# Optimization experiments

Measured on AMD Instinct MI355X. Metric: run time of the kernel, lower is better.

Reference implementation:

```python
import jax, jax.numpy as jnp
import numpy as np

N_NODES = 100000
N_EDGES = 3200000
D_IN = 128
D_OUT = 128
BN_EPS = 1e-5


def setup_inputs() -> dict:
    key = jax.random.key(0)
    k1, k2, k3, k4, k5 = jax.random.split(key, 5)
    x = jax.random.normal(k1, (N_NODES, D_IN), dtype=jnp.float32)
    edge_index = jax.random.randint(k2, (2, N_EDGES), 0, N_NODES, dtype=jnp.int64)
    s = 1.0 / np.sqrt(D_IN)
    W_l = jax.random.uniform(k3, (D_IN, D_OUT), minval=-s, maxval=s, dtype=jnp.float32)
    b_l = jnp.zeros((D_OUT,), dtype=jnp.float32)
    W_r = jax.random.uniform(k4, (D_IN, D_OUT), minval=-s, maxval=s, dtype=jnp.float32)
    gamma = jnp.ones((D_OUT,), dtype=jnp.float32)
    beta = jnp.zeros((D_OUT,), dtype=jnp.float32)
    return {"x": x, "edge_index": edge_index, "W_l": W_l, "b_l": b_l,
            "W_r": W_r, "gamma": gamma, "beta": beta}


def _sage_bn(x, edge_index, W_l, b_l, W_r, gamma, beta):
    src, dst = edge_index[0], edge_index[1]
    # gather source features, scatter-sum at targets, divide by in-degree (mean aggr)
    agg_sum = jax.ops.segment_sum(x[src], dst, num_segments=N_NODES)  # [N, D_IN]
    deg = jax.ops.segment_sum(jnp.ones((N_EDGES,), x.dtype), dst, num_segments=N_NODES)
    agg = agg_sum / jnp.maximum(deg, 1.0)[:, None]
    # SAGEConv: lin_l(aggregated) + lin_r(self)
    x_raw = agg @ W_l + b_l + x @ W_r  # [N, D_OUT]
    # BatchNorm1d (training mode: batch stats, biased variance)
    mu = jnp.mean(x_raw, axis=0)
    var = jnp.var(x_raw, axis=0)
    x_deskewed = (x_raw - mu) * jax.lax.rsqrt(var + BN_EPS) * gamma + beta
    return x_raw, x_deskewed


def reference(x, edge_index, W_l, b_l, W_r, gamma, beta):
    return _sage_bn(x, edge_index, W_l, b_l, W_r, gamma, beta)
```

## Files before the change

kernel.cpp:

```cpp
#include <hip/hip_runtime.h>

constexpr int NN = 100000;
constexpr int NE = 3200000;
constexpr int DD = 128;
constexpr int NB = 782;
constexpr int RND = 8192;
#define BN_EPS 1e-5f

typedef __attribute__((ext_vector_type(8))) short bf16x8;
typedef __attribute__((ext_vector_type(4))) float f32x4;
typedef __attribute__((ext_vector_type(2))) float f32x2;

constexpr size_t WS_CNT   = 0;
constexpr size_t WS_COFF  = 4096;
constexpr size_t WS_CUR   = 8192;
constexpr size_t WS_FLAG  = 12288;
constexpr size_t WS_BNSUM = 12800;
constexpr size_t WS_BNSQ  = 13312;
constexpr size_t WS_ZERO  = 16384;
constexpr size_t WS_DEG   = 16384;
constexpr size_t WS_OFF   = 416384;
constexpr size_t WS_CSR   = 816384;
constexpr size_t WS_WT    = 13616384;

__device__ inline unsigned bf16rne(float f) {
    unsigned u = __float_as_uint(f);
    return (u + 0x7fffu + ((u >> 16) & 1u)) >> 16;
}

#if __has_builtin(__builtin_amdgcn_cvt_pk_f32_fp8)
__device__ inline f32x2 fp8pk_lo(unsigned u) {
    return __builtin_amdgcn_cvt_pk_f32_fp8((int)u, false);
}
__device__ inline f32x2 fp8pk_hi(unsigned u) {
    return __builtin_amdgcn_cvt_pk_f32_fp8((int)u, true);
}
__device__ inline unsigned f32x4_to_fp8(float4 v) {
    int w = __builtin_amdgcn_cvt_pk_fp8_f32(v.x, v.y, 0, false);
    w = __builtin_amdgcn_cvt_pk_fp8_f32(v.z, v.w, w, true);
    return (unsigned)w;
}
#else
__device__ inline float fp8_to_f32_1(unsigned b) {
    unsigned s = (b & 0x80u) << 24;
    unsigned em = b & 0x7fu;
    float f;
    if (em >= 8) f = __uint_as_float((em << 20) + (120u << 23));
    else f = (float)em * 0.001953125f;
    return __uint_as_float(__float_as_uint(f) | s);
}
__device__ inline f32x2 fp8pk_lo(unsigned u) {
    f32x2 r;
    r[0] = fp8_to_f32_1(u & 0xffu);
    r[1] = fp8_to_f32_1((u >> 8) & 0xffu);
    return r;
}
__device__ inline f32x2 fp8pk_hi(unsigned u) {
    f32x2 r;
    r[0] = fp8_to_f32_1((u >> 16) & 0xffu);
    r[1] = fp8_to_f32_1((u >> 24) & 0xffu);
    return r;
}
__device__ inline unsigned f32_to_fp8_1(float f) {
    unsigned s = (__float_as_uint(f) >> 24) & 0x80u;
    float a = fabsf(f);
    if (!(a > 0.f)) return s;
    if (a >= 448.f) return s | 0x7Eu;
    int e = (int)(__float_as_uint(a) >> 23) - 127;
    if (e < -6) e = -6;
    float step = __uint_as_float((unsigned)(e - 3 + 127) << 23);
    int m = (int)rintf(a / step);
    if (m >= 16) { e += 1; m = 8; }
    if (m >= 8) return s | (unsigned)((e + 7) << 3) | (unsigned)(m - 8);
    return s | (unsigned)m;
}
__device__ inline unsigned f32x4_to_fp8(float4 v) {
    return f32_to_fp8_1(v.x) | (f32_to_fp8_1(v.y) << 8) |
           (f32_to_fp8_1(v.z) << 16) | (f32_to_fp8_1(v.w) << 24);
}
#endif

#define ACC8(u)                                                              \
    {                                                                        \
        aa0 += fp8pk_lo((u).x);                                              \
        aa1 += fp8pk_hi((u).x);                                              \
        aa2 += fp8pk_lo((u).y);                                              \
        aa3 += fp8pk_hi((u).y);                                              \
    }

__global__ void k_detect(const int* __restrict__ ei, int* __restrict__ flag) {
    int lane = threadIdx.x;
    int v = ei[2 * lane + 1];
    unsigned long long b = __ballot(v == 0);
    if (lane == 0) *flag = (b == ~0ull) ? 1 : 0;
}

__global__ __launch_bounds__(256) void k_prep(const float* __restrict__ x,
                                              unsigned* __restrict__ xb,
                                              unsigned* __restrict__ xq,
                                              const float* __restrict__ Wl,
                                              const float* __restrict__ Wr,
                                              unsigned short* __restrict__ Wt) {
    int bid = blockIdx.x;
    if (bid < 2048) {
        int total = NN * DD / 4;
        for (int i = bid * 256 + threadIdx.x; i < total; i += 2048 * 256) {
            float4 v = ((const float4*)x)[i];
            unsigned a = (bf16rne(v.y) << 16) | bf16rne(v.x);
            unsigned b = (bf16rne(v.w) << 16) | bf16rne(v.z);
            ((uint2*)xb)[i] = make_uint2(a, b);
            xq[i] = f32x4_to_fp8(v);
        }
    } else {
        int idx = (bid - 2048) * 256 + threadIdx.x;
        int n = idx >> 8, k = idx & 255;
        float v = (k < 128) ? Wl[(size_t)k * DD + n] : Wr[(size_t)(k - 128) * DD + n];
        Wt[idx] = (unsigned short)bf16rne(v);
    }
}

__global__ __launch_bounds__(256) void k_bcount(const int* __restrict__ ei,
                                                const int* __restrict__ flag,
                                                int* __restrict__ cnt) {
    __shared__ int hist[NB];
    for (int i = threadIdx.x; i < NB; i += 256) hist[i] = 0;
    __syncthreads();
    int i64 = *flag;
    int stride = gridDim.x * 256;
    if (i64) {
        const int4* dp = (const int4*)(ei + 2 * (size_t)NE);
        int total = NE / 2;
        for (int i = blockIdx.x * 256 + threadIdx.x; i < total; i += stride) {
            int4 v = dp[i];
            atomicAdd(&hist[v.x >> 7], 1);
            atomicAdd(&hist[v.z >> 7], 1);
        }
    } else {
        const int4* dp = (const int4*)(ei + (size_t)NE);
        int total = NE / 4;
        for (int i = blockIdx.x * 256 + threadIdx.x; i < total; i += stride) {
            int4 v = dp[i];
            atomicAdd(&hist[v.x >> 7], 1);
            atomicAdd(&hist[v.y >> 7], 1);
            atomicAdd(&hist[v.z >> 7], 1);
            atomicAdd(&hist[v.w >> 7], 1);
        }
    }
    __syncthreads();
    for (int i = threadIdx.x; i < NB; i += 256) {
        int c = hist[i];
        if (c) atomicAdd(&cnt[i], c);
    }
}

__global__ __launch_bounds__(256) void k_scan(const int* __restrict__ cnt,
                                              int* __restrict__ coff,
                                              int* __restrict__ cur) {
    __shared__ int s[NB];
    for (int i = threadIdx.x; i < NB; i += 256) s[i] = cnt[i];
    __syncthreads();
    if (threadIdx.x == 0) {
        int acc = 0;
        for (int i = 0; i < NB; ++i) { int c = s[i]; s[i] = acc; acc += c; }
    }
    __syncthreads();
    for (int i = threadIdx.x; i < NB; i += 256) { coff[i] = s[i]; cur[i] = s[i]; }
    if (threadIdx.x == 0) coff[NB] = NE;
}

__global__ __launch_bounds__(256) void k_bin(const int* __restrict__ ei,
                                             const int* __restrict__ flag,
                                             int* __restrict__ cur,
                                             unsigned* __restrict__ bin) {
    __shared__ int hist[NB];
    __shared__ int sbs[NB];
    __shared__ int gbase[NB];
    __shared__ int rk[NB];
    __shared__ int wsum[256];
    __shared__ unsigned short sj[RND];
    int tid = threadIdx.x;
    for (int i = tid; i < NB; i += 256) { hist[i] = 0; rk[i] = 0; }
    __syncthreads();
    int i64 = *flag;
    int e0 = blockIdx.x * RND;
    int cntE = NE - e0; if (cntE > RND) cntE = RND;

    for (int j = tid; j < cntE; j += 256) {
        int e = e0 + j;
        int dst = i64 ? ei[2 * (NE + e)] : ei[NE + e];
        atomicAdd(&hist[dst >> 7], 1);
    }
    __syncthreads();

    int b4 = tid * 4;
    int l0 = (b4 + 0 < NB) ? hist[b4 + 0] : 0;
    int l1 = (b4 + 1 < NB) ? hist[b4 + 1] : 0;
    int l2 = (b4 + 2 < NB) ? hist[b4 + 2] : 0;
    int l3 = (b4 + 3 < NB) ? hist[b4 + 3] : 0;
    int tsum = l0 + l1 + l2 + l3;
    wsum[tid] = tsum;
    __syncthreads();
    for (int d = 1; d < 256; d <<= 1) {
        int v = (tid >= d) ? wsum[tid - d] : 0;
        __syncthreads();
        wsum[tid] += v;
        __syncthreads();
    }
    int p = wsum[tid] - tsum;
    if (b4 + 0 < NB) sbs[b4 + 0] = p;
    if (b4 + 1 < NB) sbs[b4 + 1] = p + l0;
    if (b4 + 2 < NB) sbs[b4 + 2] = p + l0 + l1;
    if (b4 + 3 < NB) sbs[b4 + 3] = p + l0 + l1 + l2;
    __syncthreads();

    for (int j = tid; j < cntE; j += 256) {
        int e = e0 + j;
        int dst = i64 ? ei[2 * (NE + e)] : ei[NE + e];
        int b = dst >> 7;
        int r = atomicAdd(&rk[b], 1);
        sj[sbs[b] + r] = (unsigned short)j;
    }
    for (int b = tid; b < NB; b += 256) {
        int c = hist[b];
        if (c > 0) gbase[b] = atomicAdd(&cur[b], c);
    }
    __syncthreads();

    for (int t = tid; t < cntE; t += 256) {
        int j = sj[t];
        int e = e0 + j;
        int src = i64 ? ei[2 * e] : ei[e];
        int dst = i64 ? ei[2 * (NE + e)] : ei[NE + e];
        int b = dst >> 7;
        bin[gbase[b] + (t - sbs[b])] = ((unsigned)src << 7) | (unsigned)(dst & 127);
    }
}

__global__ __launch_bounds__(256) void k_csr(const unsigned* __restrict__ bin,
                                             const int* __restrict__ coff,
                                             int* __restrict__ csr,
                                             int* __restrict__ deg,
                                             int* __restrict__ off) {
    __shared__ int hist[128];
    __shared__ int sb[128];
    __shared__ int curs[128];
    int b = blockIdx.x;
    int tid = threadIdx.x;
    if (tid < 128) hist[tid] = 0;
    __syncthreads();
    int e0 = coff[b], e1 = coff[b + 1];
    for (int j = e0 + tid; j < e1; j += 256)
        atomicAdd(&hist[bin[j] & 127], 1);
    __syncthreads();
    if (tid == 0) {
        int acc = 0;
        for (int i = 0; i < 128; ++i) { sb[i] = acc; acc += hist[i]; }
    }
    __syncthreads();
    if (tid < 128) curs[tid] = sb[tid];
    __syncthreads();
    for (int j = e0 + tid; j < e1; j += 256) {
        unsigned p = bin[j];
        int d = p & 127;
        int r = atomicAdd(&curs[d], 1);
        csr[e0 + r] = (int)((p >> 7) << 4);
    }
    int n = b * 128 + tid;
    if (tid < 128 && n < NN) {
        deg[n] = hist[tid];
        off[n] = e0 + sb[tid];
    }
}

__global__ __launch_bounds__(256) void k_agg(const uint2* __restrict__ xq2,
                                             const int* __restrict__ csr,
                                             const int* __restrict__ deg,
                                             const int* __restrict__ off,
                                             unsigned* __restrict__ aggb) {
    int w = (blockIdx.x * 256 + threadIdx.x) >> 6;
    int lane = threadIdx.x & 63;
    if (w >= NN) return;
    int dg = deg[w];
    int o = off[w];
    int q = lane >> 4;
    int cl = lane & 15;
    const uint2* xp = xq2 + cl;
    f32x2 aa0 = {0.f, 0.f}, aa1 = {0.f, 0.f}, aa2 = {0.f, 0.f}, aa3 = {0.f, 0.f};

    int j = 0;
    for (; j + 16 <= dg; j += 16) {
        int s0 = csr[o + j + q];
        int s1 = csr[o + j + 4 + q];
        int s2 = csr[o + j + 8 + q];
        int s3 = csr[o + j + 12 + q];
        uint2 u0 = xp[s0];
        uint2 u1 = xp[s1];
        uint2 u2 = xp[s2];
        uint2 u3 = xp[s3];
        ACC8(u0); ACC8(u1); ACC8(u2); ACC8(u3);
    }
    for (; j + 4 <= dg; j += 4) {
        int s = csr[o + j + q];
        uint2 u = xp[s];
        ACC8(u);
    }
    int rem = dg - j;
    if (q < rem) {
        int s = csr[o + j + q];
        uint2 u = xp[s];
        ACC8(u);
    }

    float a0 = aa0[0], a1 = aa0[1], a2 = aa1[0], a3 = aa1[1];
    float a4 = aa2[0], a5 = aa2[1], a6 = aa3[0], a7 = aa3[1];
    a0 += __shfl_xor(a0, 16); a0 += __shfl_xor(a0, 32);
    a1 += __shfl_xor(a1, 16); a1 += __shfl_xor(a1, 32);
    a2 += __shfl_xor(a2, 16); a2 += __shfl_xor(a2, 32);
    a3 += __shfl_xor(a3, 16); a3 += __shfl_xor(a3, 32);
    a4 += __shfl_xor(a4, 16); a4 += __shfl_xor(a4, 32);
    a5 += __shfl_xor(a5, 16); a5 += __shfl_xor(a5, 32);
    a6 += __shfl_xor(a6, 16); a6 += __shfl_xor(a6, 32);
    a7 += __shfl_xor(a7, 16); a7 += __shfl_xor(a7, 32);

    if (lane < 16) {
        float inv = 1.0f / fmaxf((float)dg, 1.0f);
        uint4 p;
        p.x = (bf16rne(a1 * inv) << 16) | bf16rne(a0 * inv);
        p.y = (bf16rne(a3 * inv) << 16) | bf16rne(a2 * inv);
        p.z = (bf16rne(a5 * inv) << 16) | bf16rne(a4 * inv);
        p.w = (bf16rne(a7 * inv) << 16) | bf16rne(a6 * inv);
        ((uint4*)aggb)[(size_t)w * 16 + cl] = p;
    }
}

__global__ __launch_bounds__(256) void k_gemm(const unsigned short* __restrict__ aggb,
                                              const unsigned short* __restrict__ xb,
                                              const unsigned short* __restrict__ Wt,
                                              const float* __restrict__ bl,
                                              float* __restrict__ out_raw,
                                              float* __restrict__ bn_sum,
                                              float* __restrict__ bn_sq) {
    __shared__ unsigned short sW[128][264];
    __shared__ float s_s[4][128];
    __shared__ float s_q[4][128];
    int tid = threadIdx.x;
    int wv = tid >> 6, lane = tid & 63;
    int l15 = lane & 15, lhi = lane >> 4;
    int mr = blockIdx.x * 128 + wv * 32;

    {
        const uint4* g = (const uint4*)Wt;
        #pragma unroll
        for (int it = 0; it < 16; ++it) {
            int c = tid + it * 256;
            int row = c >> 5;
            int col = (c & 31) * 8;
            *(uint4*)&sW[row][col] = g[c];
        }
    }

    int r0 = mr + l15;       if (r0 > NN - 1) r0 = NN - 1;
    int r1 = mr + 16 + l15;  if (r1 > NN - 1) r1 = NN - 1;
    const unsigned short* a0p = aggb + (size_t)r0 * DD;
    const unsigned short* a1p = aggb + (size_t)r1 * DD;
    const unsigned short* x0p = xb + (size_t)r0 * DD;
    const unsigned short* x1p = xb + (size_t)r1 * DD;

    bf16x8 A0[8], A1[8];
    #pragma unroll
    for (int ks = 0; ks < 8; ++ks) {
        int kk = (ks & 3) * 32 + lhi * 8;
        if (ks < 4) {
            A0[ks] = *(const bf16x8*)(a0p + kk);
            A1[ks] = *(const bf16x8*)(a1p + kk);
        } else {
            A0[ks] = *(const bf16x8*)(x0p + kk);
            A1[ks] = *(const bf16x8*)(x1p + kk);
        }
    }

    f32x4 acc[2][8];
    #pragma unroll
    for (int m = 0; m < 2; ++m)
        #pragma unroll
        for (int nt = 0; nt < 8; ++nt)
            acc[m][nt] = (f32x4){0.f, 0.f, 0.f, 0.f};

    __syncthreads();

    #pragma unroll
    for (int ks = 0; ks < 8; ++ks) {
        #pragma unroll
        for (int nt = 0; nt < 8; ++nt) {
            bf16x8 b = *(const bf16x8*)&sW[nt * 16 + l15][ks * 32 + lhi * 8];
            acc[0][nt] = __builtin_amdgcn_mfma_f32_16x16x32_bf16(A0[ks], b, acc[0][nt], 0, 0, 0);
            acc[1][nt] = __builtin_amdgcn_mfma_f32_16x16x32_bf16(A1[ks], b, acc[1][nt], 0, 0, 0);
        }
    }

    float bias8[8];
    #pragma unroll
    for (int nt = 0; nt < 8; ++nt) bias8[nt] = bl[nt * 16 + l15];

    float s8[8] = {}, q8[8] = {};
    #pragma unroll
    for (int m = 0; m < 2; ++m) {
        #pragma unroll
        for (int r = 0; r < 4; ++r) {
            int row = mr + m * 16 + lhi * 4 + r;
            if (row < NN) {
                #pragma unroll
                for (int nt = 0; nt < 8; ++nt) {
                    float v = acc[m][nt][r] + bias8[nt];
                    out_raw[(size_t)row * DD + nt * 16 + l15] = v;
                    s8[nt] += v;
                    q8[nt] += v * v;
                }
            }
        }
    }

    #pragma unroll
    for (int nt = 0; nt < 8; ++nt) {
        s8[nt] += __shfl_xor(s8[nt], 16);
        s8[nt] += __shfl_xor(s8[nt], 32);
        q8[nt] += __shfl_xor(q8[nt], 16);
        q8[nt] += __shfl_xor(q8[nt], 32);
    }
    if (lhi == 0) {
        #pragma unroll
        for (int nt = 0; nt < 8; ++nt) {
            s_s[wv][nt * 16 + l15] = s8[nt];
            s_q[wv][nt * 16 + l15] = q8[nt];
        }
    }
    __syncthreads();
    if (tid < 128) {
        float ts = s_s[0][tid] + s_s[1][tid] + s_s[2][tid] + s_s[3][tid];
        float tq = s_q[0][tid] + s_q[1][tid] + s_q[2][tid] + s_q[3][tid];
        atomicAdd(&bn_sum[tid], ts);
        atomicAdd(&bn_sq[tid], tq);
    }
}

__global__ __launch_bounds__(256) void k_norm(const float* __restrict__ raw,
                                              const float* __restrict__ bn_sum,
                                              const float* __restrict__ bn_sq,
                                              const float* __restrict__ gamma,
                                              const float* __restrict__ beta,
                                              float* __restrict__ out) {
    const float invN = 1.0f / (float)NN;
    int total = NN * DD / 4;
    for (int idx = blockIdx.x * 256 + threadIdx.x; idx < total; idx += gridDim.x * 256) {
        int cp = idx & 31;
        float4 v = ((const float4*)raw)[idx];
        float4 s = ((const float4*)bn_sum)[cp];
        float4 q = ((const float4*)bn_sq)[cp];
        float4 g = ((const float4*)gamma)[cp];
        float4 b = ((const float4*)beta)[cp];
        float4 o;
        { float mu = s.x * invN; float var = q.x * invN - mu * mu;
          o.x = (v.x - mu) * rsqrtf(var + BN_EPS) * g.x + b.x; }
        { float mu = s.y * invN; float var = q.y * invN - mu * mu;
          o.y = (v.y - mu) * rsqrtf(var + BN_EPS) * g.y + b.y; }
        { float mu = s.z * invN; float var = q.z * invN - mu * mu;
          o.z = (v.z - mu) * rsqrtf(var + BN_EPS) * g.z + b.z; }
        { float mu = s.w * invN; float var = q.w * invN - mu * mu;
          o.w = (v.w - mu) * rsqrtf(var + BN_EPS) * g.w + b.w; }
        ((float4*)out)[idx] = o;
    }
}

extern "C" void kernel_launch(void* const* d_in, const int* in_sizes, int n_in,
                              void* d_out, int out_size, void* d_ws, size_t ws_size,
                              hipStream_t stream) {
    const float* x     = (const float*)d_in[0];
    const int*   ei    = (const int*)d_in[1];
    const float* Wl    = (const float*)d_in[2];
    const float* bl    = (const float*)d_in[3];
    const float* Wr    = (const float*)d_in[4];
    const float* gamma = (const float*)d_in[5];
    const float* beta  = (const float*)d_in[6];

    float* out_raw = (float*)d_out;
    float* out_bn  = out_raw + (size_t)NN * DD;
    unsigned* xq   = (unsigned*)d_out;
    unsigned* bin  = (unsigned*)out_bn;
    unsigned* aggb = (unsigned*)out_bn;
    unsigned* xb   = (unsigned*)((char*)out_bn + (size_t)NN * DD * 2);

    char* ws = (char*)d_ws;
    int*   cnt    = (int*)(ws + WS_CNT);
    int*   coff   = (int*)(ws + WS_COFF);
    int*   cur    = (int*)(ws + WS_CUR);
    int*   flag   = (int*)(ws + WS_FLAG);
    float* bn_sum = (float*)(ws + WS_BNSUM);
    float* bn_sq  = (float*)(ws + WS_BNSQ);
    int*   deg    = (int*)(ws + WS_DEG);
    int*   off    = (int*)(ws + WS_OFF);
    int*   csr    = (int*)(ws + WS_CSR);
    unsigned short* Wt = (unsigned short*)(ws + WS_WT);

    hipMemsetAsync(d_ws, 0, WS_ZERO, stream);

    k_detect<<<1, 64, 0, stream>>>(ei, flag);
    k_prep<<<2048 + 128, 256, 0, stream>>>(x, xb, xq, Wl, Wr, Wt);
    k_bcount<<<512, 256, 0, stream>>>(ei, flag, cnt);
    k_scan<<<1, 256, 0, stream>>>(cnt, coff, cur);
    k_bin<<<(NE + RND - 1) / RND, 256, 0, stream>>>(ei, flag, cur, bin);
    k_csr<<<NB, 256, 0, stream>>>(bin, coff, csr, deg, off);
    k_agg<<<(NN * 64 + 255) / 256, 256, 0, stream>>>((const uint2*)xq, csr, deg, off, aggb);
    k_gemm<<<(NN + 127) / 128, 256, 0, stream>>>((const unsigned short*)aggb,
                                                 (const unsigned short*)xb,
                                                 Wt, bl, out_raw, bn_sum, bn_sq);
    k_norm<<<4096, 256, 0, stream>>>(out_raw, bn_sum, bn_sq, gamma, beta, out_bn);
}
```

Measured before the change: 225.7 us.

## Replace atomic bucket counting with per-block histogram matrix and column scan

The binning stage now records a per-block histogram matrix instead of global atomic counts, then a column-wise prefix scan computes a deterministic global base for every block and bucket. The second binning pass reuses the stored histogram, so it no longer re-reads destinations for counting and no longer needs atomics on a global cursor. This gives a stable edge order and removes one pass over the edge array, at the cost of an extra kernel launch and a 391x782 matrix written into scratch space inside the output buffer.

```diff
diff --git a/kernel.cpp b/kernel.cpp
--- a/kernel.cpp
+++ b/kernel.cpp
@@ -5,6 +5,7 @@
 constexpr int DD = 128;
 constexpr int NB = 782;
 constexpr int RND = 8192;
+constexpr int NBLK = 391;
 #define BN_EPS 1e-5f
 
 typedef __attribute__((ext_vector_type(8))) short bf16x8;
@@ -13,7 +14,6 @@
 
 constexpr size_t WS_CNT   = 0;
 constexpr size_t WS_COFF  = 4096;
-constexpr size_t WS_CUR   = 8192;
 constexpr size_t WS_FLAG  = 12288;
 constexpr size_t WS_BNSUM = 12800;
 constexpr size_t WS_BNSQ  = 13312;
@@ -119,27 +119,29 @@
     }
 }
 
-__global__ __launch_bounds__(256) void k_bcount(const int* __restrict__ ei,
-                                                const int* __restrict__ flag,
-                                                int* __restrict__ cnt) {
+__global__ __launch_bounds__(256) void k_binA(const int* __restrict__ ei,
+                                              const int* __restrict__ flag,
+                                              int* __restrict__ cntM) {
     __shared__ int hist[NB];
-    for (int i = threadIdx.x; i < NB; i += 256) hist[i] = 0;
+    int tid = threadIdx.x;
+    for (int i = tid; i < NB; i += 256) hist[i] = 0;
     __syncthreads();
     int i64 = *flag;
-    int stride = gridDim.x * 256;
+    int e0 = blockIdx.x * RND;
+    int cntE = NE - e0; if (cntE > RND) cntE = RND;
     if (i64) {
-        const int4* dp = (const int4*)(ei + 2 * (size_t)NE);
-        int total = NE / 2;
-        for (int i = blockIdx.x * 256 + threadIdx.x; i < total; i += stride) {
-            int4 v = dp[i];
+        const int4* dp = (const int4*)(ei + 2 * (size_t)NE + 2 * (size_t)e0);
+        int total = cntE >> 1;
+        for (int k = tid; k < total; k += 256) {
+            int4 v = dp[k];
             atomicAdd(&hist[v.x >> 7], 1);
             atomicAdd(&hist[v.z >> 7], 1);
         }
     } else {
-        const int4* dp = (const int4*)(ei + (size_t)NE);
-        int total = NE / 4;
-        for (int i = blockIdx.x * 256 + threadIdx.x; i < total; i += stride) {
-            int4 v = dp[i];
+        const int4* dp = (const int4*)(ei + (size_t)NE + e0);
+        int total = cntE >> 2;
+        for (int k = tid; k < total; k += 256) {
+            int4 v = dp[k];
             atomicAdd(&hist[v.x >> 7], 1);
             atomicAdd(&hist[v.y >> 7], 1);
             atomicAdd(&hist[v.z >> 7], 1);
@@ -147,15 +149,31 @@
         }
     }
     __syncthreads();
-    for (int i = threadIdx.x; i < NB; i += 256) {
-        int c = hist[i];
-        if (c) atomicAdd(&cnt[i], c);
-    }
+    size_t base = (size_t)blockIdx.x * NB;
+    for (int i = tid; i < NB; i += 256) cntM[base + i] = hist[i];
+}
+
+__global__ __launch_bounds__(512) void k_colscan(const int* __restrict__ cntM,
+                                                 int* __restrict__ gbR,
+                                                 int* __restrict__ cnt) {
+    __shared__ int s[512];
+    int b = blockIdx.x;
+    int tid = threadIdx.x;
+    int v = (tid < NBLK) ? cntM[(size_t)tid * NB + b] : 0;
+    s[tid] = v;
+    __syncthreads();
+    for (int d = 1; d < 512; d <<= 1) {
+        int t = (tid >= d) ? s[tid - d] : 0;
+        __syncthreads();
+        s[tid] += t;
+        __syncthreads();
+    }
+    if (tid < NBLK) gbR[(size_t)tid * NB + b] = s[tid] - v;
+    if (tid == NBLK - 1) cnt[b] = s[tid];
 }
 
 __global__ __launch_bounds__(256) void k_scan(const int* __restrict__ cnt,
-                                              int* __restrict__ coff,
-                                              int* __restrict__ cur) {
+                                              int* __restrict__ coff) {
     __shared__ int s[NB];
     for (int i = threadIdx.x; i < NB; i += 256) s[i] = cnt[i];
     __syncthreads();
@@ -164,14 +182,16 @@
         for (int i = 0; i < NB; ++i) { int c = s[i]; s[i] = acc; acc += c; }
     }
     __syncthreads();
-    for (int i = threadIdx.x; i < NB; i += 256) { coff[i] = s[i]; cur[i] = s[i]; }
+    for (int i = threadIdx.x; i < NB; i += 256) coff[i] = s[i];
     if (threadIdx.x == 0) coff[NB] = NE;
 }
 
-__global__ __launch_bounds__(256) void k_bin(const int* __restrict__ ei,
-                                             const int* __restrict__ flag,
-                                             int* __restrict__ cur,
-                                             unsigned* __restrict__ bin) {
+__global__ __launch_bounds__(256) void k_binB(const int* __restrict__ ei,
+                                              const int* __restrict__ flag,
+                                              const int* __restrict__ cntM,
+                                              const int* __restrict__ gbR,
+                                              const int* __restrict__ coff,
+                                              unsigned* __restrict__ bin) {
     __shared__ int hist[NB];
     __shared__ int sbs[NB];
     __shared__ int gbase[NB];
@@ -179,18 +199,16 @@
     __shared__ int wsum[256];
     __shared__ unsigned short sj[RND];
     int tid = threadIdx.x;
-    for (int i = tid; i < NB; i += 256) { hist[i] = 0; rk[i] = 0; }
+    size_t mrow = (size_t)blockIdx.x * NB;
+    for (int i = tid; i < NB; i += 256) {
+        hist[i] = cntM[mrow + i];
+        gbase[i] = coff[i] + gbR[mrow + i];
+        rk[i] = 0;
+    }
     __syncthreads();
     int i64 = *flag;
     int e0 = blockIdx.x * RND;
     int cntE = NE - e0; if (cntE > RND) cntE = RND;
-
-    for (int j = tid; j < cntE; j += 256) {
-        int e = e0 + j;
-        int dst = i64 ? ei[2 * (NE + e)] : ei[NE + e];
-        atomicAdd(&hist[dst >> 7], 1);
-    }
-    __syncthreads();
 
     int b4 = tid * 4;
     int l0 = (b4 + 0 < NB) ? hist[b4 + 0] : 0;
@@ -219,10 +237,6 @@
         int b = dst >> 7;
         int r = atomicAdd(&rk[b], 1);
         sj[sbs[b] + r] = (unsigned short)j;
-    }
-    for (int b = tid; b < NB; b += 256) {
-        int c = hist[b];
-        if (c > 0) gbase[b] = atomicAdd(&cur[b], c);
     }
     __syncthreads();
 
@@ -485,6 +499,8 @@
     float* out_raw = (float*)d_out;
     float* out_bn  = out_raw + (size_t)NN * DD;
     unsigned* xq   = (unsigned*)d_out;
+    int*      cntM = (int*)((char*)d_out + 16000000);
+    int*      gbR  = (int*)((char*)d_out + 20000000);
     unsigned* bin  = (unsigned*)out_bn;
     unsigned* aggb = (unsigned*)out_bn;
     unsigned* xb   = (unsigned*)((char*)out_bn + (size_t)NN * DD * 2);
@@ -492,7 +508,6 @@
     char* ws = (char*)d_ws;
     int*   cnt    = (int*)(ws + WS_CNT);
     int*   coff   = (int*)(ws + WS_COFF);
-    int*   cur    = (int*)(ws + WS_CUR);
     int*   flag   = (int*)(ws + WS_FLAG);
     float* bn_sum = (float*)(ws + WS_BNSUM);
     float* bn_sq  = (float*)(ws + WS_BNSQ);
@@ -505,9 +520,10 @@
 
     k_detect<<<1, 64, 0, stream>>>(ei, flag);
     k_prep<<<2048 + 128, 256, 0, stream>>>(x, xb, xq, Wl, Wr, Wt);
-    k_bcount<<<512, 256, 0, stream>>>(ei, flag, cnt);
-    k_scan<<<1, 256, 0, stream>>>(cnt, coff, cur);
-    k_bin<<<(NE + RND - 1) / RND, 256, 0, stream>>>(ei, flag, cur, bin);
+    k_binA<<<NBLK, 256, 0, stream>>>(ei, flag, cntM);
+    k_colscan<<<NB, 512, 0, stream>>>(cntM, gbR, cnt);
+    k_scan<<<1, 256, 0, stream>>>(cnt, coff);
+    k_binB<<<NBLK, 256, 0, stream>>>(ei, flag, cntM, gbR, coff, bin);
     k_csr<<<NB, 256, 0, stream>>>(bin, coff, csr, deg, off);
     k_agg<<<(NN * 64 + 255) / 256, 256, 0, stream>>>((const uint2*)xq, csr, deg, off, aggb);
     k_gemm<<<(NN + 127) / 128, 256, 0, stream>>>((const unsigned short*)aggb,
```

After: 212.0 us. -6.1%, faster.
